# Optimization experiments

Hardware: AMD Instinct MI355X
Metric: run time of the kernel (lower is better)

The kernel has to match this reference:

```python
import jax, jax.numpy as jnp
import numpy as np

B, S, HMODEL = 2, 4096, 2048
NH, HD, K = 16, 128, 4
RMS_EPS = 1e-5
L2_EPS = 1e-6


def setup_inputs() -> dict:
    key = jax.random.key(0)
    ks = jax.random.split(key, 10)
    def p(k, shape, std=0.02):
        return jax.random.normal(k, shape, jnp.float32) * std
    return {
        "x": jax.random.normal(ks[0], (B, S, HMODEL), jnp.float32),
        "Wq": p(ks[1], (NH * HD, HMODEL)),
        "Wk": p(ks[2], (NH * HD, HMODEL)),
        "Wv": p(ks[3], (NH * HD, HMODEL)),
        "Wb": p(ks[4], (NH, HMODEL)),
        "Wo": p(ks[5], (HMODEL, NH * HD)),
        "conv_q": p(ks[6], (NH * HD, K), 0.3),
        "conv_k": p(ks[7], (NH * HD, K), 0.3),
        "conv_v": p(ks[8], (NH * HD, K), 0.3),
        "rms_w": jnp.ones((HD,), jnp.float32),
    }


def causal_conv_silu(x, w):
    # depthwise causal conv1d: x [B,S,C], w [C,K]; out[t] = sum_i w[:,i]*x[t-K+1+i]
    Kw = w.shape[1]
    xp = jnp.pad(x, ((0, 0), (Kw - 1, 0), (0, 0)))
    out = sum(w[:, i] * xp[:, i:i + x.shape[1], :] for i in range(Kw))
    return jax.nn.silu(out)


def l2norm(x):
    return x * jax.lax.rsqrt(jnp.sum(x * x, axis=-1, keepdims=True) + L2_EPS)


def reference(x, Wq, Wk, Wv, Wb, Wo, conv_q, conv_k, conv_v, rms_w):
    b, s, _ = x.shape
    nh = Wb.shape[0]
    hd = Wq.shape[0] // nh

    q = causal_conv_silu(x @ Wq.T, conv_q)
    k = causal_conv_silu(x @ Wk.T, conv_k)
    v = causal_conv_silu(x @ Wv.T, conv_v)

    q = q.reshape(b, s, nh, hd)
    k = k.reshape(b, s, nh, hd)
    v = v.reshape(b, s, nh, hd)
    beta = jax.nn.sigmoid(x @ Wb.T)  # [B,S,NH]

    # qk l2 norm in kernel + default scale d_k^-0.5 on q
    q = l2norm(q) * (hd ** -0.5)
    k = l2norm(k)

    # delta rule recurrence: state [B,NH,HD,HD] (d_k x d_v)
    qT = jnp.moveaxis(q, 1, 0)  # [S,B,NH,HD]
    kT = jnp.moveaxis(k, 1, 0)
    vT = jnp.moveaxis(v, 1, 0)
    bT = jnp.moveaxis(beta, 1, 0)  # [S,B,NH]

    def step(state, inp):
        qt, kt, vt, bt = inp
        pred = jnp.einsum('bhd,bhdv->bhv', kt, state)
        delta = bt[..., None] * (vt - pred)
        state = state + jnp.einsum('bhd,bhv->bhdv', kt, delta)
        ot = jnp.einsum('bhd,bhdv->bhv', qt, state)
        return state, ot

    s0 = jnp.zeros((b, nh, hd, hd), x.dtype)
    _, o = jax.lax.scan(step, s0, (qT, kT, vT, bT))
    o = jnp.moveaxis(o, 0, 1)  # [B,S,NH,HD]

    # RMSNorm over head_dim
    o = o * jax.lax.rsqrt(jnp.mean(o * o, axis=-1, keepdims=True) + RMS_EPS) * rms_w

    o = o.reshape(b, s, nh * hd) @ Wo.T
    return o
```

## Files before the change

### kernel.cpp

```cpp
#include <hip/hip_runtime.h>

#define DI __device__ __forceinline__

constexpr int Bb = 2, Ss = 4096, Hm = 2048, NHh = 16, HDd = 128;
constexpr int ROWS = Bb * Ss;
constexpr int QKVN = 3 * Hm;
constexpr int CC = 64;
constexpr int NC = Ss / CC;

typedef __bf16 bf16x8 __attribute__((ext_vector_type(8)));
typedef float f32x4 __attribute__((ext_vector_type(4)));

DI unsigned short f2bf(float f) {
  unsigned int u = __float_as_uint(f);
  u = u + 0x7FFFu + ((u >> 16) & 1u);
  return (unsigned short)(u >> 16);
}
DI float bf2f(unsigned int u) { return __uint_as_float(u << 16); }
DI void ld_bf8(const unsigned short* p, float* f) {
  uint4 u = *(const uint4*)p;
  f[0] = bf2f(u.x & 0xffffu); f[1] = bf2f(u.x >> 16);
  f[2] = bf2f(u.y & 0xffffu); f[3] = bf2f(u.y >> 16);
  f[4] = bf2f(u.z & 0xffffu); f[5] = bf2f(u.z >> 16);
  f[6] = bf2f(u.w & 0xffffu); f[7] = bf2f(u.w >> 16);
}

DI void gld16(const unsigned short* g, unsigned short* l) {
  __builtin_amdgcn_global_load_lds(
      (const __attribute__((address_space(1))) unsigned int*)g,
      (__attribute__((address_space(3))) unsigned int*)l, 16, 0, 0);
}

DI void bar_lds() {
  asm volatile("s_waitcnt lgkmcnt(0)" ::: "memory");
  __builtin_amdgcn_s_barrier();
}

__global__ void cast_x_k(const float* __restrict__ x, unsigned short* __restrict__ xb) {
  int i = blockIdx.x * 256 + threadIdx.x;
  float4 f = ((const float4*)x)[i];
  ushort4 u;
  u.x = f2bf(f.x); u.y = f2bf(f.y); u.z = f2bf(f.z); u.w = f2bf(f.w);
  ((ushort4*)xb)[i] = u;
}

__global__ void cast_w_k(const float* __restrict__ Wq, const float* __restrict__ Wk,
                         const float* __restrict__ Wv, const float* __restrict__ Wo,
                         unsigned short* __restrict__ wqkv, unsigned short* __restrict__ wo) {
  const int W1 = Hm * Hm;
  int idx = blockIdx.x * 256 + threadIdx.x;
  for (int r = 0; r < 4; r++) {
    int i = idx + r * W1;
    if (i < W1)            wqkv[i] = f2bf(Wq[i]);
    else if (i < 2 * W1)   wqkv[i] = f2bf(Wk[i - W1]);
    else if (i < 3 * W1)   wqkv[i] = f2bf(Wv[i - 2 * W1]);
    else                   wo[i - 3 * W1] = f2bf(Wo[i - 3 * W1]);
  }
}

DI bf16x8 ldsw(const unsigned short* base, int r, int c16) {
  return *(const bf16x8*)&base[r * 64 + ((c16 ^ (r & 7)) << 3)];
}

template <bool BF16_OUT>
__global__ __launch_bounds__(512) void gemm256(const unsigned short* __restrict__ A,
                                               const unsigned short* __restrict__ Bm,
                                               void* __restrict__ Cout,
                                               int M, int N, int Kd) {
  __shared__ __align__(16) unsigned short As[3][16384];
  __shared__ __align__(16) unsigned short Bs[2][16384];
  int tid = threadIdx.x;
  int wave = tid >> 6, lane = tid & 63;
  int lm = lane & 15, lq = lane >> 4;
  int wm = (wave >> 2) * 128, wn = (wave & 3) * 64;

  int nx = N >> 8;
  int nwg = gridDim.x * gridDim.y;
  int lin = blockIdx.x + gridDim.x * blockIdx.y;
  int cpx = nwg >> 3;
  int swz = (lin & 7) * cpx + (lin >> 3);
  int bn = (swz % nx) << 8, bm = (swz / nx) << 8;

  int NT = Kd >> 6;
  int rsub = lane >> 3;
  int csw = ((lane & 7) ^ rsub) << 3;

  auto stageA = [&](int buf, int half, int ts) {
    int ksrc = (ts < NT ? ts : NT - 1) << 6;
#pragma unroll
    for (int i = 0; i < 2; i++) {
      int blk = wave * 2 + i;
      int r = half * 128 + blk * 8 + rsub;
      gld16(&A[(size_t)(bm + r) * Kd + ksrc + csw], &As[buf][half * 8192 + blk * 512]);
    }
  };
  auto stageB = [&](int buf, int half, int ts) {
    int ksrc = (ts < NT ? ts : NT - 1) << 6;
#pragma unroll
    for (int i = 0; i < 2; i++) {
      int blk = wave * 2 + i;
      int r = half * 128 + blk * 8 + rsub;
      gld16(&Bm[(size_t)(bn + r) * Kd + ksrc + csw], &Bs[buf][half * 8192 + blk * 512]);
    }
  };

  f32x4 acc[8][4] = {};
  bf16x8 a[4][2], b[4][2];

  stageA(0, 0, 0); stageA(0, 1, 0); stageB(0, 0, 0); stageB(0, 1, 0);
  stageA(1, 0, 1); stageA(1, 1, 1); stageB(1, 0, 1); stageB(1, 1, 1);
  asm volatile("s_waitcnt vmcnt(8)" ::: "memory");
  __builtin_amdgcn_s_barrier();

  int cur_a = 0, cur_b = 0;
  for (int t = 0; t < NT; t++) {
    const unsigned short* Ac = As[cur_a];
    const unsigned short* Bc = Bs[cur_b];
    int ap2 = cur_a == 0 ? 2 : cur_a - 1;

#pragma unroll
    for (int fi = 0; fi < 4; fi++)
#pragma unroll
      for (int kk = 0; kk < 2; kk++)
        a[fi][kk] = ldsw(Ac, wm + fi * 16 + lm, kk * 4 + lq);
#pragma unroll
    for (int fj = 0; fj < 2; fj++)
#pragma unroll
      for (int kk = 0; kk < 2; kk++)
        b[fj][kk] = ldsw(Bc, wn + fj * 16 + lm, kk * 4 + lq);
    stageA(ap2, 0, t + 2);
    asm volatile("" ::: "memory");
    __builtin_amdgcn_s_barrier();
    asm volatile("s_waitcnt lgkmcnt(0)" ::: "memory");
    __builtin_amdgcn_sched_barrier(0);
    __builtin_amdgcn_s_setprio(1);
#pragma unroll
    for (int kk = 0; kk < 2; kk++)
#pragma unroll
      for (int fi = 0; fi < 4; fi++)
#pragma unroll
        for (int fj = 0; fj < 2; fj++)
          acc[fi][fj] = __builtin_amdgcn_mfma_f32_16x16x32_bf16(a[fi][kk], b[fj][kk], acc[fi][fj], 0, 0, 0);
    __builtin_amdgcn_s_setprio(0);
    asm volatile("" ::: "memory");
    __builtin_amdgcn_s_barrier();

#pragma unroll
    for (int fj = 0; fj < 2; fj++)
#pragma unroll
      for (int kk = 0; kk < 2; kk++)
        b[2 + fj][kk] = ldsw(Bc, wn + (2 + fj) * 16 + lm, kk * 4 + lq);
    stageA(ap2, 1, t + 2);
    asm volatile("" ::: "memory");
    __builtin_amdgcn_s_barrier();
    asm volatile("s_waitcnt lgkmcnt(0)" ::: "memory");
    __builtin_amdgcn_sched_barrier(0);
    __builtin_amdgcn_s_setprio(1);
#pragma unroll
    for (int kk = 0; kk < 2; kk++)
#pragma unroll
      for (int fi = 0; fi < 4; fi++)
#pragma unroll
        for (int fj = 0; fj < 2; fj++)
          acc[fi][2 + fj] = __builtin_amdgcn_mfma_f32_16x16x32_bf16(a[fi][kk], b[2 + fj][kk], acc[fi][2 + fj], 0, 0, 0);
    __builtin_amdgcn_s_setprio(0);
    asm volatile("" ::: "memory");
    __builtin_amdgcn_s_barrier();

#pragma unroll
    for (int fi = 0; fi < 4; fi++)
#pragma unroll
      for (int kk = 0; kk < 2; kk++)
        a[fi][kk] = ldsw(Ac, wm + 64 + fi * 16 + lm, kk * 4 + lq);
    stageB(cur_b, 0, t + 2);
    asm volatile("" ::: "memory");
    __builtin_amdgcn_s_barrier();
    asm volatile("s_waitcnt lgkmcnt(0)" ::: "memory");
    __builtin_amdgcn_sched_barrier(0);
    __builtin_amdgcn_s_setprio(1);
#pragma unroll
    for (int kk = 0; kk < 2; kk++)
#pragma unroll
      for (int fi = 0; fi < 4; fi++)
#pragma unroll
        for (int fj = 0; fj < 2; fj++)
          acc[4 + fi][2 + fj] = __builtin_amdgcn_mfma_f32_16x16x32_bf16(a[fi][kk], b[2 + fj][kk], acc[4 + fi][2 + fj], 0, 0, 0);
    __builtin_amdgcn_s_setprio(0);
    asm volatile("" ::: "memory");
    __builtin_amdgcn_s_barrier();

    stageB(cur_b, 1, t + 2);
    asm volatile("" ::: "memory");
    __builtin_amdgcn_s_barrier();
    __builtin_amdgcn_s_setprio(1);
#pragma unroll
    for (int kk = 0; kk < 2; kk++)
#pragma unroll
      for (int fi = 0; fi < 4; fi++)
#pragma unroll
        for (int fj = 0; fj < 2; fj++)
          acc[4 + fi][fj] = __builtin_amdgcn_mfma_f32_16x16x32_bf16(a[fi][kk], b[fj][kk], acc[4 + fi][fj], 0, 0, 0);
    __builtin_amdgcn_s_setprio(0);
    asm volatile("s_waitcnt vmcnt(8)" ::: "memory");
    __builtin_amdgcn_s_barrier();

    cur_a = cur_a == 2 ? 0 : cur_a + 1;
    cur_b ^= 1;
  }

#pragma unroll
  for (int fi = 0; fi < 8; fi++)
#pragma unroll
    for (int fj = 0; fj < 4; fj++) {
      int row = bm + wm + fi * 16 + lq * 4;
      int col = bn + wn + fj * 16 + lm;
#pragma unroll
      for (int r = 0; r < 4; r++) {
        if (BF16_OUT)
          ((unsigned short*)Cout)[(size_t)(row + r) * N + col] = f2bf(acc[fi][fj][r]);
        else
          ((float*)Cout)[(size_t)(row + r) * N + col] = acc[fi][fj][r];
      }
    }
}

__global__ __launch_bounds__(256) void conv_k(const unsigned short* __restrict__ qkvh,
                                              const float* __restrict__ cwq,
                                              const float* __restrict__ cwk,
                                              const float* __restrict__ cwv,
                                              unsigned short* __restrict__ qb,
                                              unsigned short* __restrict__ kb,
                                              unsigned short* __restrict__ vb) {
  __shared__ __align__(16) float sm[32 * 260];
  __shared__ float fac[64];
  int tid = threadIdx.x;
  int cblk = blockIdx.x * 256;
  int s0 = blockIdx.y * 32;
  int z = blockIdx.z;
  int sel = z >> 1, b = z & 1;
  const float* cw = sel == 0 ? cwq : (sel == 1 ? cwk : cwv);
  int c = cblk + tid;
  float4 w = ((const float4*)cw)[c];
  const unsigned short* in = qkvh + (size_t)b * Ss * QKVN + sel * Hm + c;
  float x0 = (s0 >= 3) ? bf2f(in[(size_t)(s0 - 3) * QKVN]) : 0.f;
  float x1 = (s0 >= 2) ? bf2f(in[(size_t)(s0 - 2) * QKVN]) : 0.f;
  float x2 = (s0 >= 1) ? bf2f(in[(size_t)(s0 - 1) * QKVN]) : 0.f;
  for (int si = 0; si < 32; si++) {
    float x3 = bf2f(in[(size_t)(s0 + si) * QKVN]);
    float a = w.x * x0 + w.y * x1 + w.z * x2 + w.w * x3;
    sm[si * 260 + tid] = a / (1.f + __expf(-a));
    x0 = x1; x1 = x2; x2 = x3;
  }
  __syncthreads();
  if (sel < 2) {
    int si = tid >> 3, p = tid & 7;
    const float* row = &sm[si * 260 + p * 32];
    float ss = 0.f;
#pragma unroll
    for (int j = 0; j < 32; j += 4) {
      float4 v4 = *(const float4*)(row + j);
      ss += v4.x * v4.x + v4.y * v4.y + v4.z * v4.z + v4.w * v4.w;
    }
    ss += __shfl_xor(ss, 1);
    ss += __shfl_xor(ss, 2);
    float f = rsqrtf(ss + 1e-6f);
    if (sel == 0) f *= 0.08838834764831845f;
    if ((p & 3) == 0) fac[si * 2 + (p >> 2)] = f;
  }
  __syncthreads();
  unsigned short* outp = sel == 0 ? qb : (sel == 1 ? kb : vb);
  int hl = tid >> 7;
  for (int si = 0; si < 32; si++) {
    float val = sm[si * 260 + tid];
    if (sel < 2) val *= fac[si * 2 + hl];
    outp[(size_t)(b * Ss + s0 + si) * Hm + cblk + tid] = f2bf(val);
  }
}

__global__ __launch_bounds__(256) void beta_k(const float* __restrict__ x,
                                              const float* __restrict__ Wbm,
                                              float* __restrict__ beta) {
  int wid = threadIdx.x >> 6, lane = threadIdx.x & 63;
  int row = blockIdx.x * 4 + wid;
  int h = lane & 15, part = lane >> 4;
  const float* xr = x + (size_t)row * Hm + part * 512;
  const float* wr = Wbm + (size_t)h * Hm + part * 512;
  float acc = 0.f;
  for (int j = 0; j < 512; j += 4) {
    float4 xv = *(const float4*)(xr + j);
    float4 wv = *(const float4*)(wr + j);
    acc += xv.x * wv.x + xv.y * wv.y + xv.z * wv.z + xv.w * wv.w;
  }
  acc += __shfl_xor(acc, 16);
  acc += __shfl_xor(acc, 32);
  if (part == 0) beta[(size_t)row * NHh + h] = 1.f / (1.f + __expf(-acc));
}

__global__ __launch_bounds__(256) void recA_k(const unsigned short* __restrict__ qg,
                                              unsigned short* kg,
                                              const unsigned short* __restrict__ vg,
                                              const float* __restrict__ beta,
                                              unsigned short* __restrict__ Wo_,
                                              unsigned short* __restrict__ Uo,
                                              unsigned short* __restrict__ Kto) {
  __shared__ __align__(16) unsigned short Kc[64 * 136];
  __shared__ __align__(16) unsigned short Qc[64 * 136];
  __shared__ __align__(16) unsigned short Vt[128 * 72];
  __shared__ __align__(16) unsigned short Kt[128 * 72];
  __shared__ __align__(16) unsigned short Xa[64 * 72], Xat[64 * 72];
  __shared__ __align__(16) unsigned short Xb2[64 * 72], Xbt[64 * 72];
  __shared__ __align__(16) unsigned short Pa[64 * 72], Pb[64 * 72];
  __shared__ float bl[64];
  int tid = threadIdx.x;
  int c = blockIdx.x, bh = blockIdx.y;
  int b = bh >> 4, h = bh & 15;
  size_t cid = (size_t)bh * NC + c;
  size_t rowbase = (size_t)b * Ss + (size_t)c * CC;
  int wave = tid >> 6, lane = tid & 63, lm = lane & 15, lq = lane >> 4;

  for (int idx = tid; idx < 1024; idx += 256) {
    int r = idx >> 4, c8 = (idx & 15) * 8;
    *(uint4*)&Kc[r * 136 + c8] = *(const uint4*)&kg[(rowbase + r) * Hm + h * HDd + c8];
    *(uint4*)&Qc[r * 136 + c8] = *(const uint4*)&qg[(rowbase + r) * Hm + h * HDd + c8];
  }
  for (int idx = tid; idx < 8192; idx += 256) {
    int s = idx >> 7, vv = idx & 127;
    Vt[vv * 72 + s] = vg[(rowbase + s) * Hm + h * HDd + vv];
  }
  if (tid < 64) bl[tid] = beta[(rowbase + tid) * NHh + h];
  __syncthreads();

  for (int idx = tid; idx < 8192; idx += 256) {
    int s = idx >> 7, d = idx & 127;
    Kt[d * 72 + s] = Kc[s * 136 + d];
  }
  {
    f32x4 accA[4] = {};
#pragma unroll
    for (int kk = 0; kk < 4; kk++) {
      bf16x8 af = *(const bf16x8*)&Kc[(wave * 16 + lm) * 136 + kk * 32 + lq * 8];
#pragma unroll
      for (int st = 0; st < 4; st++) {
        bf16x8 bfr = *(const bf16x8*)&Kc[(st * 16 + lm) * 136 + kk * 32 + lq * 8];
        accA[st] = __builtin_amdgcn_mfma_f32_16x16x32_bf16(af, bfr, accA[st], 0, 0, 0);
      }
    }
#pragma unroll
    for (int st = 0; st < 4; st++)
#pragma unroll
      for (int r = 0; r < 4; r++) {
        int t = wave * 16 + lq * 4 + r, s = st * 16 + lm;
        float m = (t > s) ? -bl[t] * accA[st][r] : 0.f;
        unsigned short mb = f2bf(m);
        Xa[t * 72 + s] = mb;
        Xat[s * 72 + t] = mb;
        Pa[t * 72 + s] = (t == s) ? f2bf(1.f) : mb;
      }
  }
  {
    f32x4 accQ[4] = {};
#pragma unroll
    for (int kk = 0; kk < 4; kk++) {
      bf16x8 af = *(const bf16x8*)&Qc[(wave * 16 + lm) * 136 + kk * 32 + lq * 8];
#pragma unroll
      for (int st = 0; st < 4; st++) {
        bf16x8 bfr = *(const bf16x8*)&Kc[(st * 16 + lm) * 136 + kk * 32 + lq * 8];
        accQ[st] = __builtin_amdgcn_mfma_f32_16x16x32_bf16(af, bfr, accQ[st], 0, 0, 0);
      }
    }
#pragma unroll
    for (int st = 0; st < 4; st++)
#pragma unroll
      for (int r = 0; r < 4; r++) {
        int t = wave * 16 + lq * 4 + r, s = st * 16 + lm;
        kg[(rowbase + t) * Hm + h * HDd + s] = (s <= t) ? f2bf(accQ[st][r]) : (unsigned short)0;
      }
  }
  __syncthreads();

  unsigned short *X = Xa, *Xt = Xat, *Xn = Xb2, *Xnt = Xbt, *P = Pa, *Pn = Pb;
  for (int lvl = 1; lvl <= 5; lvl++) {
    f32x4 a1[4] = {}, a2[4] = {};
#pragma unroll
    for (int kk = 0; kk < 2; kk++) {
      bf16x8 afx  = *(const bf16x8*)&X[(wave * 16 + lm) * 72 + kk * 32 + lq * 8];
      bf16x8 afxt = *(const bf16x8*)&Xt[(wave * 16 + lm) * 72 + kk * 32 + lq * 8];
#pragma unroll
      for (int st = 0; st < 4; st++) {
        bf16x8 bx  = *(const bf16x8*)&X[(st * 16 + lm) * 72 + kk * 32 + lq * 8];
        bf16x8 bxt = *(const bf16x8*)&Xt[(st * 16 + lm) * 72 + kk * 32 + lq * 8];
        a1[st] = __builtin_amdgcn_mfma_f32_16x16x32_bf16(afx, bxt, a1[st], 0, 0, 0);
        a2[st] = __builtin_amdgcn_mfma_f32_16x16x32_bf16(afxt, bx, a2[st], 0, 0, 0);
      }
    }
#pragma unroll
    for (int st = 0; st < 4; st++)
#pragma unroll
      for (int r = 0; r < 4; r++) {
        int t = wave * 16 + lq * 4 + r, s = st * 16 + lm;
        Xn[t * 72 + s]  = f2bf(a1[st][r]);
        Xnt[t * 72 + s] = f2bf(a2[st][r]);
      }
    __syncthreads();
    f32x4 ap[4];
#pragma unroll
    for (int st = 0; st < 4; st++)
#pragma unroll
      for (int r = 0; r < 4; r++)
        ap[st][r] = bf2f(P[(wave * 16 + lq * 4 + r) * 72 + st * 16 + lm]);
#pragma unroll
    for (int kk = 0; kk < 2; kk++) {
      bf16x8 afp = *(const bf16x8*)&P[(wave * 16 + lm) * 72 + kk * 32 + lq * 8];
#pragma unroll
      for (int st = 0; st < 4; st++) {
        bf16x8 bxnt = *(const bf16x8*)&Xnt[(st * 16 + lm) * 72 + kk * 32 + lq * 8];
        ap[st] = __builtin_amdgcn_mfma_f32_16x16x32_bf16(afp, bxnt, ap[st], 0, 0, 0);
      }
    }
#pragma unroll
    for (int st = 0; st < 4; st++)
#pragma unroll
      for (int r = 0; r < 4; r++) {
        int t = wave * 16 + lq * 4 + r, s = st * 16 + lm;
        Pn[t * 72 + s] = f2bf((lvl == 5) ? ap[st][r] * bl[s] : ap[st][r]);
      }
    unsigned short* tmp;
    tmp = X; X = Xn; Xn = tmp;
    tmp = Xt; Xt = Xnt; Xnt = tmp;
    tmp = P; P = Pn; Pn = tmp;
    __syncthreads();
  }

  for (int idx = tid; idx < 1024; idx += 256) {
    int d = idx >> 3, s8 = (idx & 7) * 8;
    *(uint4*)&Kto[cid * 8192 + d * 64 + s8] = *(const uint4*)&Kt[d * 72 + s8];
  }
  {
    unsigned short* Up = Uo + cid * 8192;
    unsigned short* Wp = Wo_ + cid * 8192;
    f32x4 accU[8] = {}, accW[8] = {};
#pragma unroll
    for (int kk = 0; kk < 2; kk++) {
      bf16x8 af = *(const bf16x8*)&P[(wave * 16 + lm) * 72 + kk * 32 + lq * 8];
#pragma unroll
      for (int nt = 0; nt < 8; nt++) {
        bf16x8 bv = *(const bf16x8*)&Vt[(nt * 16 + lm) * 72 + kk * 32 + lq * 8];
        bf16x8 bk = *(const bf16x8*)&Kt[(nt * 16 + lm) * 72 + kk * 32 + lq * 8];
        accU[nt] = __builtin_amdgcn_mfma_f32_16x16x32_bf16(af, bv, accU[nt], 0, 0, 0);
        accW[nt] = __builtin_amdgcn_mfma_f32_16x16x32_bf16(af, bk, accW[nt], 0, 0, 0);
      }
    }
#pragma unroll
    for (int nt = 0; nt < 8; nt++)
#pragma unroll
      for (int r = 0; r < 4; r++) {
        int t = wave * 16 + lq * 4 + r, n = nt * 16 + lm;
        Up[t * 128 + n] = f2bf(accU[nt][r]);
        Wp[t * 128 + n] = f2bf(accW[nt][r]);
      }
  }
}

__global__ __launch_bounds__(256) void recB_k(const unsigned short* __restrict__ qg,
                                              const unsigned short* __restrict__ atg,
                                              const unsigned short* __restrict__ Wg,
                                              const unsigned short* __restrict__ Ug,
                                              const unsigned short* __restrict__ Ktg,
                                              unsigned short* __restrict__ og) {
  __shared__ __align__(16) unsigned short Wc[64 * 136];
  __shared__ __align__(16) unsigned short Qc[64 * 136];
  __shared__ __align__(16) unsigned short Ktc[128 * 72];
  __shared__ __align__(16) unsigned short Atc[64 * 72];
  __shared__ __align__(16) unsigned short Uc[64 * 24];
  __shared__ __align__(16) unsigned short Dt[16 * 72];
  __shared__ __align__(16) unsigned short Stb[16 * 136];
  __shared__ float St32[16 * 132];
  int tid = threadIdx.x;
  int lin = blockIdx.x + (blockIdx.y << 3);
  int xcd = lin & 7, slot = lin >> 3;
  int vs = slot & 7;
  int bh = xcd + ((slot >> 3) << 3);
  int b = bh >> 4, h = bh & 15, v0 = vs * 16;
  int wave = tid >> 6, lane = tid & 63, lm = lane & 15, lq = lane >> 4;

  for (int i = tid; i < 16 * 132; i += 256) St32[i] = 0.f;
  for (int i = tid; i < 16 * 136; i += 256) Stb[i] = 0;

  {
    size_t cid0 = (size_t)bh * NC;
    size_t rb0 = (size_t)b * Ss;
    const unsigned short* Wp = Wg + cid0 * 8192;
    const unsigned short* Ktp = Ktg + cid0 * 8192;
    const unsigned short* Up = Ug + cid0 * 8192 + v0;
#pragma unroll
    for (int j = 0; j < 4; j++) {
      int idx = tid + j * 256;
      int r = idx >> 4, c8 = (idx & 15) * 8;
      *(uint4*)&Wc[r * 136 + c8] = *(const uint4*)&Wp[r * 128 + c8];
      *(uint4*)&Qc[r * 136 + c8] = *(const uint4*)&qg[(rb0 + r) * Hm + h * HDd + c8];
      int r2 = idx >> 3, d8 = (idx & 7) * 8;
      *(uint4*)&Ktc[r2 * 72 + d8] = *(const uint4*)&Ktp[r2 * 64 + d8];
    }
#pragma unroll
    for (int j = 0; j < 2; j++) {
      int idx = tid + j * 256;
      int t = idx >> 3, s8 = (idx & 7) * 8;
      *(uint4*)&Atc[t * 72 + s8] = *(const uint4*)&atg[(rb0 + t) * Hm + h * HDd + s8];
    }
    if (tid < 128) {
      int t = tid >> 1, c8 = (tid & 1) * 8;
      *(uint4*)&Uc[t * 24 + c8] = *(const uint4*)&Up[t * 128 + c8];
    }
  }
  __syncthreads();

  for (int c = 0; c < NC; c++) {
    size_t rb = (size_t)b * Ss + (size_t)c * CC;
    int cn = (c + 1 < NC) ? c + 1 : c;
    size_t cidn = (size_t)bh * NC + cn;
    size_t rbn = (size_t)b * Ss + (size_t)cn * CC;
    const unsigned short* Wpn = Wg + cidn * 8192;
    const unsigned short* Ktpn = Ktg + cidn * 8192;
    const unsigned short* Upn = Ug + cidn * 8192 + v0;
    uint4 pw[4], pq[4], pk[4], pa[2], pu;
#pragma unroll
    for (int j = 0; j < 4; j++) {
      int idx = tid + j * 256;
      int r = idx >> 4, c8 = (idx & 15) * 8;
      pw[j] = *(const uint4*)&Wpn[r * 128 + c8];
      pq[j] = *(const uint4*)&qg[(rbn + r) * Hm + h * HDd + c8];
      int r2 = idx >> 3, d8 = (idx & 7) * 8;
      pk[j] = *(const uint4*)&Ktpn[r2 * 64 + d8];
    }
#pragma unroll
    for (int j = 0; j < 2; j++) {
      int idx = tid + j * 256;
      int t = idx >> 3, s8 = (idx & 7) * 8;
      pa[j] = *(const uint4*)&atg[(rbn + t) * Hm + h * HDd + s8];
    }
    if (tid < 128) {
      int t = tid >> 1, c8 = (tid & 1) * 8;
      pu = *(const uint4*)&Upn[t * 128 + c8];
    }

    {
      f32x4 accD = {};
#pragma unroll
      for (int kk = 0; kk < 4; kk++) {
        bf16x8 af = *(const bf16x8*)&Wc[(wave * 16 + lm) * 136 + kk * 32 + lq * 8];
        bf16x8 bfr = *(const bf16x8*)&Stb[lm * 136 + kk * 32 + lq * 8];
        accD = __builtin_amdgcn_mfma_f32_16x16x32_bf16(af, bfr, accD, 0, 0, 0);
      }
#pragma unroll
      for (int r = 0; r < 4; r++) {
        int t = wave * 16 + lq * 4 + r;
        float dv = bf2f(Uc[t * 24 + lm]) - accD[r];
        Dt[lm * 72 + t] = f2bf(dv);
      }
    }
    bar_lds();

    f32x4 accO = {};
    f32x4 accP[2] = {};
    {
#pragma unroll
      for (int kk = 0; kk < 4; kk++) {
        bf16x8 af = *(const bf16x8*)&Qc[(wave * 16 + lm) * 136 + kk * 32 + lq * 8];
        bf16x8 bfr = *(const bf16x8*)&Stb[lm * 136 + kk * 32 + lq * 8];
        accO = __builtin_amdgcn_mfma_f32_16x16x32_bf16(af, bfr, accO, 0, 0, 0);
      }
#pragma unroll
      for (int kk = 0; kk < 2; kk++) {
        bf16x8 af = *(const bf16x8*)&Atc[(wave * 16 + lm) * 72 + kk * 32 + lq * 8];
        bf16x8 bfr = *(const bf16x8*)&Dt[lm * 72 + kk * 32 + lq * 8];
        accO = __builtin_amdgcn_mfma_f32_16x16x32_bf16(af, bfr, accO, 0, 0, 0);
        bf16x8 afd = *(const bf16x8*)&Dt[lm * 72 + kk * 32 + lq * 8];
#pragma unroll
        for (int j = 0; j < 2; j++) {
          int dt = wave * 2 + j;
          bf16x8 bk = *(const bf16x8*)&Ktc[(dt * 16 + lm) * 72 + kk * 32 + lq * 8];
          accP[j] = __builtin_amdgcn_mfma_f32_16x16x32_bf16(afd, bk, accP[j], 0, 0, 0);
        }
      }
    }
    bar_lds();

#pragma unroll
    for (int r = 0; r < 4; r++) {
      int t = wave * 16 + lq * 4 + r;
      og[(rb + t) * Hm + h * HDd + v0 + lm] = f2bf(accO[r]);
    }
#pragma unroll
    for (int j = 0; j < 2; j++) {
      int dt = wave * 2 + j;
#pragma unroll
      for (int r = 0; r < 4; r++) {
        int vv = lq * 4 + r, d = dt * 16 + lm;
        float ns = St32[vv * 132 + d] + accP[j][r];
        St32[vv * 132 + d] = ns;
        Stb[vv * 136 + d] = f2bf(ns);
      }
    }
#pragma unroll
    for (int j = 0; j < 4; j++) {
      int idx = tid + j * 256;
      int r = idx >> 4, c8 = (idx & 15) * 8;
      *(uint4*)&Wc[r * 136 + c8] = pw[j];
      *(uint4*)&Qc[r * 136 + c8] = pq[j];
      int r2 = idx >> 3, d8 = (idx & 7) * 8;
      *(uint4*)&Ktc[r2 * 72 + d8] = pk[j];
    }
#pragma unroll
    for (int j = 0; j < 2; j++) {
      int idx = tid + j * 256;
      int t = idx >> 3, s8 = (idx & 7) * 8;
      *(uint4*)&Atc[t * 72 + s8] = pa[j];
    }
    if (tid < 128) {
      int t = tid >> 1, c8 = (tid & 1) * 8;
      *(uint4*)&Uc[t * 24 + c8] = pu;
    }
    bar_lds();
  }
}

__global__ __launch_bounds__(256) void rmsn_k(const unsigned short* __restrict__ o,
                                              const float* __restrict__ rw,
                                              unsigned short* __restrict__ ob) {
  int tid = threadIdx.x;
  size_t rowoff = (size_t)blockIdx.x * Hm + tid * 8;
  float f[8];
  ld_bf8(o + rowoff, f);
  float ss = f[0]*f[0] + f[1]*f[1] + f[2]*f[2] + f[3]*f[3] +
             f[4]*f[4] + f[5]*f[5] + f[6]*f[6] + f[7]*f[7];
  ss += __shfl_xor(ss, 1); ss += __shfl_xor(ss, 2); ss += __shfl_xor(ss, 4); ss += __shfl_xor(ss, 8);
  float sc = rsqrtf(ss * (1.f / 128.f) + 1e-5f);
  int d = (tid & 15) * 8;
  float4 wa = *(const float4*)(rw + d);
  float4 wb = *(const float4*)(rw + d + 4);
  ushort4 u0, u1;
  u0.x = f2bf(f[0] * sc * wa.x); u0.y = f2bf(f[1] * sc * wa.y);
  u0.z = f2bf(f[2] * sc * wa.z); u0.w = f2bf(f[3] * sc * wa.w);
  u1.x = f2bf(f[4] * sc * wb.x); u1.y = f2bf(f[5] * sc * wb.y);
  u1.z = f2bf(f[6] * sc * wb.z); u1.w = f2bf(f[7] * sc * wb.w);
  ((ushort4*)ob)[rowoff / 4] = u0;
  ((ushort4*)ob)[rowoff / 4 + 1] = u1;
}

extern "C" void kernel_launch(void* const* d_in, const int* in_sizes, int n_in,
                              void* d_out, int out_size, void* d_ws, size_t ws_size,
                              hipStream_t stream) {
  const float* x  = (const float*)d_in[0];
  const float* Wq = (const float*)d_in[1];
  const float* Wk = (const float*)d_in[2];
  const float* Wv = (const float*)d_in[3];
  const float* Wb = (const float*)d_in[4];
  const float* Wo = (const float*)d_in[5];
  const float* cq = (const float*)d_in[6];
  const float* ck = (const float*)d_in[7];
  const float* cv = (const float*)d_in[8];
  const float* rw = (const float*)d_in[9];

  unsigned short* xb  = (unsigned short*)d_out;
  unsigned short* vb  = (unsigned short*)d_out + (size_t)ROWS * Hm;
  unsigned short* o_b = (unsigned short*)d_out;
  float* out = (float*)d_out;

  char* ws = (char*)d_ws;
  size_t off = 0;
  auto alloc = [&](size_t bytes) {
    void* p = ws + off;
    off = (off + bytes + 255) & ~(size_t)255;
    return p;
  };
  unsigned short* wqkv = (unsigned short*)alloc((size_t)QKVN * Hm * 2);
  unsigned short* wob  = (unsigned short*)alloc((size_t)Hm * Hm * 2);
  unsigned short* qkvh = (unsigned short*)alloc((size_t)ROWS * QKVN * 2);
  unsigned short* qb   = (unsigned short*)alloc((size_t)ROWS * Hm * 2);
  unsigned short* kb   = (unsigned short*)alloc((size_t)ROWS * Hm * 2);
  float* beta          = (float*)alloc((size_t)ROWS * NHh * 4);
  unsigned short* Wch = qkvh;
  unsigned short* Uch = qkvh + (size_t)2048 * 8192;
  unsigned short* Kth = qkvh + (size_t)2 * 2048 * 8192;
  unsigned short* obb = qkvh;

  cast_x_k<<<ROWS * Hm / 1024, 256, 0, stream>>>(x, xb);
  cast_w_k<<<Hm * Hm / 256, 256, 0, stream>>>(Wq, Wk, Wv, Wo, wqkv, wob);
  gemm256<true><<<dim3(QKVN / 256, ROWS / 256), 512, 0, stream>>>(xb, wqkv, qkvh, ROWS, QKVN, Hm);
  beta_k<<<ROWS / 4, 256, 0, stream>>>(x, Wb, beta);
  conv_k<<<dim3(Hm / 256, Ss / 32, Bb * 3), 256, 0, stream>>>(qkvh, cq, ck, cv, qb, kb, vb);
  recA_k<<<dim3(NC, 32), 256, 0, stream>>>(qb, kb, vb, beta, Wch, Uch, Kth);
  recB_k<<<dim3(8, 32), 256, 0, stream>>>(qb, kb, Wch, Uch, Kth, o_b);
  rmsn_k<<<ROWS, 256, 0, stream>>>(o_b, rw, obb);
  gemm256<false><<<dim3(Hm / 256, ROWS / 256), 512, 0, stream>>>(obb, wob, out, ROWS, Hm, Hm);
}
```

Baseline: 920.3 us.

## Software-pipeline LDS fragment loads across MFMA phases in the GEMM main loop

```diff
diff --git a/kernel.cpp b/kernel.cpp
--- a/kernel.cpp
+++ b/kernel.cpp
@@ -111,30 +111,37 @@
   stageA(1, 0, 1); stageA(1, 1, 1); stageB(1, 0, 1); stageB(1, 1, 1);
   asm volatile("s_waitcnt vmcnt(8)" ::: "memory");
   __builtin_amdgcn_s_barrier();
+#pragma unroll
+  for (int fi = 0; fi < 4; fi++)
+#pragma unroll
+    for (int kk = 0; kk < 2; kk++)
+      a[fi][kk] = ldsw(As[0], wm + fi * 16 + lm, kk * 4 + lq);
+#pragma unroll
+  for (int fj = 0; fj < 2; fj++)
+#pragma unroll
+    for (int kk = 0; kk < 2; kk++)
+      b[fj][kk] = ldsw(Bs[0], wn + fj * 16 + lm, kk * 4 + lq);
 
   int cur_a = 0, cur_b = 0;
   for (int t = 0; t < NT; t++) {
     const unsigned short* Ac = As[cur_a];
     const unsigned short* Bc = Bs[cur_b];
+    int nxt_a = cur_a == 2 ? 0 : cur_a + 1;
+    const unsigned short* An = As[nxt_a];
+    const unsigned short* Bn = Bs[cur_b ^ 1];
     int ap2 = cur_a == 0 ? 2 : cur_a - 1;
 
-#pragma unroll
-    for (int fi = 0; fi < 4; fi++)
-#pragma unroll
-      for (int kk = 0; kk < 2; kk++)
-        a[fi][kk] = ldsw(Ac, wm + fi * 16 + lm, kk * 4 + lq);
-#pragma unroll
-    for (int fj = 0; fj < 2; fj++)
-#pragma unroll
-      for (int kk = 0; kk < 2; kk++)
-        b[fj][kk] = ldsw(Bc, wn + fj * 16 + lm, kk * 4 + lq);
-    stageA(ap2, 0, t + 2);
     asm volatile("" ::: "memory");
     __builtin_amdgcn_s_barrier();
     asm volatile("s_waitcnt lgkmcnt(0)" ::: "memory");
     __builtin_amdgcn_sched_barrier(0);
     __builtin_amdgcn_s_setprio(1);
 #pragma unroll
+    for (int fj = 0; fj < 2; fj++)
+#pragma unroll
+      for (int kk = 0; kk < 2; kk++)
+        b[2 + fj][kk] = ldsw(Bc, wn + (2 + fj) * 16 + lm, kk * 4 + lq);
+#pragma unroll
     for (int kk = 0; kk < 2; kk++)
 #pragma unroll
       for (int fi = 0; fi < 4; fi++)
@@ -142,37 +149,27 @@
         for (int fj = 0; fj < 2; fj++)
           acc[fi][fj] = __builtin_amdgcn_mfma_f32_16x16x32_bf16(a[fi][kk], b[fj][kk], acc[fi][fj], 0, 0, 0);
     __builtin_amdgcn_s_setprio(0);
-    asm volatile("" ::: "memory");
-    __builtin_amdgcn_s_barrier();
-
-#pragma unroll
-    for (int fj = 0; fj < 2; fj++)
-#pragma unroll
-      for (int kk = 0; kk < 2; kk++)
-        b[2 + fj][kk] = ldsw(Bc, wn + (2 + fj) * 16 + lm, kk * 4 + lq);
-    stageA(ap2, 1, t + 2);
+    stageA(ap2, 0, t + 2);
+
     asm volatile("" ::: "memory");
     __builtin_amdgcn_s_barrier();
     asm volatile("s_waitcnt lgkmcnt(0)" ::: "memory");
     __builtin_amdgcn_sched_barrier(0);
     __builtin_amdgcn_s_setprio(1);
 #pragma unroll
-    for (int kk = 0; kk < 2; kk++)
-#pragma unroll
-      for (int fi = 0; fi < 4; fi++)
+    for (int fi = 0; fi < 4; fi++) {
+#pragma unroll
+      for (int kk = 0; kk < 2; kk++)
 #pragma unroll
         for (int fj = 0; fj < 2; fj++)
           acc[fi][2 + fj] = __builtin_amdgcn_mfma_f32_16x16x32_bf16(a[fi][kk], b[2 + fj][kk], acc[fi][2 + fj], 0, 0, 0);
-    __builtin_amdgcn_s_setprio(0);
-    asm volatile("" ::: "memory");
-    __builtin_amdgcn_s_barrier();
-
-#pragma unroll
-    for (int fi = 0; fi < 4; fi++)
 #pragma unroll
       for (int kk = 0; kk < 2; kk++)
         a[fi][kk] = ldsw(Ac, wm + 64 + fi * 16 + lm, kk * 4 + lq);
-    stageB(cur_b, 0, t + 2);
+    }
+    __builtin_amdgcn_s_setprio(0);
+    stageA(ap2, 1, t + 2);
+
     asm volatile("" ::: "memory");
     __builtin_amdgcn_s_barrier();
     asm volatile("s_waitcnt lgkmcnt(0)" ::: "memory");
@@ -186,26 +183,35 @@
         for (int fj = 0; fj < 2; fj++)
           acc[4 + fi][2 + fj] = __builtin_amdgcn_mfma_f32_16x16x32_bf16(a[fi][kk], b[2 + fj][kk], acc[4 + fi][2 + fj], 0, 0, 0);
     __builtin_amdgcn_s_setprio(0);
+    stageB(cur_b, 0, t + 2);
+
     asm volatile("" ::: "memory");
     __builtin_amdgcn_s_barrier();
-
-    stageB(cur_b, 1, t + 2);
+    asm volatile("s_waitcnt vmcnt(6) lgkmcnt(0)" ::: "memory");
+    __builtin_amdgcn_sched_barrier(0);
     asm volatile("" ::: "memory");
     __builtin_amdgcn_s_barrier();
     __builtin_amdgcn_s_setprio(1);
 #pragma unroll
-    for (int kk = 0; kk < 2; kk++)
-#pragma unroll
-      for (int fi = 0; fi < 4; fi++)
+    for (int fi = 0; fi < 4; fi++) {
+#pragma unroll
+      for (int kk = 0; kk < 2; kk++)
 #pragma unroll
         for (int fj = 0; fj < 2; fj++)
           acc[4 + fi][fj] = __builtin_amdgcn_mfma_f32_16x16x32_bf16(a[fi][kk], b[fj][kk], acc[4 + fi][fj], 0, 0, 0);
+#pragma unroll
+      for (int kk = 0; kk < 2; kk++)
+        a[fi][kk] = ldsw(An, wm + fi * 16 + lm, kk * 4 + lq);
+    }
+#pragma unroll
+    for (int fj = 0; fj < 2; fj++)
+#pragma unroll
+      for (int kk = 0; kk < 2; kk++)
+        b[fj][kk] = ldsw(Bn, wn + fj * 16 + lm, kk * 4 + lq);
     __builtin_amdgcn_s_setprio(0);
-    asm volatile("s_waitcnt vmcnt(8)" ::: "memory");
-    __builtin_amdgcn_s_barrier();
-
-    cur_a = cur_a == 2 ? 0 : cur_a + 1;
-    cur_b ^= 1;
+    stageB(cur_b, 1, t + 2);
+
+    cur_a = nxt_a; cur_b ^= 1;
   }
 
 #pragma unroll
```

Measured after the change: 934.0 us. No clear change (+1.5%).
